# Kernel tuning notes

Hardware: AMD Instinct MI355X
Metric: run time of the kernel (lower is better)

Reference implementation:

```python
import jax, jax.numpy as jnp
import numpy as np

HID = 1024
NH = 4
DK = 256   # head_qk_dim
DV = 512   # head_v_dim
C = 64     # chunk size (fla default)
EPS = 1e-5
GLN = 16.0  # gate_logit_normalizer


def _xavier(key, shape, gain=2 ** (-2.5)):
    fan_in, fan_out = shape
    lim = gain * np.sqrt(6.0 / (fan_in + fan_out))
    return jax.random.uniform(key, shape, jnp.float32, -lim, lim)


def setup_inputs() -> dict:
    key = jax.random.key(0)
    ks = jax.random.split(key, 8)
    x = jax.random.normal(ks[0], (4, 2048, HID), jnp.float32)
    Wq = _xavier(ks[1], (HID, NH * DK))
    Wk = _xavier(ks[2], (HID, NH * DK))
    Wv = _xavier(ks[3], (HID, NH * DV))
    Wg = _xavier(ks[4], (HID, NH * DV))
    Wgk = _xavier(ks[5], (HID, NH))
    bgk = jnp.zeros((NH,), jnp.float32)
    Wo = _xavier(ks[6], (NH * DV, HID))
    gnorm_w = jnp.ones((DV,), jnp.float32)
    return {"x": x, "Wq": Wq, "Wk": Wk, "Wv": Wv, "Wg": Wg,
            "Wgk": Wgk, "bgk": bgk, "Wo": Wo, "gnorm_w": gnorm_w}


def _chunk_simple_gla(q, k, v, g):
    # q,k: [b,h,n,dk]; v: [b,h,n,dv]; g: [b,h,n] per-head scalar log-decay
    B, H, N, dk = q.shape
    dv = v.shape[-1]
    nc = N // C
    scale = dk ** -0.5
    q = q.reshape(B, H, nc, C, dk) * scale
    k = k.reshape(B, H, nc, C, dk)
    v = v.reshape(B, H, nc, C, dv)
    g = g.reshape(B, H, nc, C)
    gc = jnp.cumsum(g, axis=-1)          # inclusive within-chunk cumulative decay
    gt = gc[..., -1]                     # total chunk decay [b,h,nc]

    # intra-chunk: o[t] += sum_{s<=t} exp(gc_t - gc_s) (q_t.k_s) v_s
    dec = gc[..., :, None] - gc[..., None, :]              # [b,h,nc,C,C]
    mask = jnp.tril(jnp.ones((C, C), bool))
    A = jnp.einsum('bhntd,bhnsd->bhnts', q, k)
    A = A * jnp.where(mask, jnp.exp(jnp.where(mask, dec, 0.0)), 0.0)
    o_intra = jnp.einsum('bhnts,bhnsd->bhntd', A, v)

    # inter-chunk: carry state S [b,h,dk,dv] across chunks
    qs = jnp.moveaxis(q, 2, 0)
    ks_ = jnp.moveaxis(k, 2, 0)
    vs = jnp.moveaxis(v, 2, 0)
    gcs = jnp.moveaxis(gc, 2, 0)
    gts = jnp.moveaxis(gt, 2, 0)
    S0 = jnp.zeros((B, H, dk, dv), q.dtype)

    def step(S, inp):
        qc, kc, vc, gcc, gtc = inp
        o_int = jnp.einsum('bhtd,bhde->bhte', qc * jnp.exp(gcc)[..., None], S)
        kd = kc * jnp.exp(gtc[..., None] - gcc)[..., None]
        S = jnp.exp(gtc)[..., None, None] * S + jnp.einsum('bhtd,bhte->bhde', kd, vc)
        return S, o_int

    _, o_inter = jax.lax.scan(step, S0, (qs, ks_, vs, gcs, gts))
    o = o_intra + jnp.moveaxis(o_inter, 0, 2)
    return o.reshape(B, H, N, dv)


def reference(x, Wq, Wk, Wv, Wg, Wgk, bgk, Wo, gnorm_w):
    B, N, _ = x.shape
    q = (x @ Wq).reshape(B, N, NH, DK).transpose(0, 2, 1, 3)
    k = (x @ Wk).reshape(B, N, NH, DK).transpose(0, 2, 1, 3)
    v = (x @ Wv).reshape(B, N, NH, DV).transpose(0, 2, 1, 3)
    gk = (x @ Wgk + bgk).transpose(0, 2, 1)          # [b,h,n]
    gk = jax.nn.log_sigmoid(gk) / GLN
    o = _chunk_simple_gla(q, k, v, gk)               # [b,h,n,dv]
    o = o.transpose(0, 2, 1, 3)                      # [b,n,h,dv]
    g = (x @ Wg).reshape(B, N, NH, DV)
    # FusedRMSNormSwishGate: RMSNorm(o) * swish(g)
    on = o * jax.lax.rsqrt(jnp.mean(o * o, axis=-1, keepdims=True) + EPS) * gnorm_w
    o = on * (g * jax.nn.sigmoid(g))
    o = o.reshape(B, N, NH * DV)
    return o @ Wo
```

## Files before the change

### kernel.cpp

```cpp
#include <hip/hip_runtime.h>

constexpr int B_  = 4;
constexpr int N_  = 2048;
constexpr int HID_ = 1024;
constexpr int NH_ = 4;
constexpr int DK_ = 256;
constexpr int DV_ = 512;
constexpr int C_  = 64;
constexpr int NC_ = 32;
constexpr int M_  = B_ * N_;
constexpr int NSEG_ = 4;
constexpr int CSEG_ = NC_ / NSEG_;

using ushort_t = unsigned short;
typedef __attribute__((ext_vector_type(8))) short bf16x8;
typedef __attribute__((ext_vector_type(4))) float f32x4;

__device__ __forceinline__ ushort_t f2bf(float f) {
  union { float fv; unsigned u; } v; v.fv = f;
  unsigned r = v.u + 0x7FFFu + ((v.u >> 16) & 1u);
  return (ushort_t)(r >> 16);
}
__device__ __forceinline__ float bf2f(ushort_t u) {
  union { unsigned u; float f; } v; v.u = ((unsigned)u) << 16; return v.f;
}

__device__ __forceinline__ void gload_lds16(const void* g, void* l) {
  __builtin_amdgcn_global_load_lds(
      (const __attribute__((address_space(1))) unsigned int*)g,
      (__attribute__((address_space(3))) unsigned int*)l, 16, 0, 0);
}

__device__ __forceinline__ f32x4 mfma16(bf16x8 a, bf16x8 b, f32x4 c) {
  return __builtin_amdgcn_mfma_f32_16x16x32_bf16(a, b, c, 0, 0, 0);
}

template<bool BF16OUT>
__global__ __launch_bounds__(256) void gemm_mfma(
    const ushort_t* __restrict__ A, const ushort_t* __restrict__ BT,
    void* __restrict__ CV, int N, int K) {
  __shared__ ushort_t Asl[128 * 32];
  __shared__ ushort_t Bsl[128 * 32];
  const int tid = threadIdx.x;
  const int wave = tid >> 6, lane = tid & 63;
  const size_t brow = (size_t)blockIdx.y * 128;
  const size_t bcol = (size_t)blockIdx.x * 128;
  const int wr = (wave >> 1) * 64, wc = (wave & 1) * 64;

  f32x4 acc[4][4];
#pragma unroll
  for (int m = 0; m < 4; ++m)
#pragma unroll
    for (int n = 0; n < 4; ++n) acc[m][n] = f32x4{0.f, 0.f, 0.f, 0.f};

  const int kk   = (lane & 3) * 8;
  const int frow = lane & 15;
  const int fk   = (lane >> 4) * 8;

  for (int k0 = 0; k0 < K; k0 += 32) {
#pragma unroll
    for (int j = 0; j < 2; ++j) {
      const int cbase = j * 4 + wave;
      const int row   = (cbase * 64 + lane) >> 2;
      gload_lds16(A  + (brow + row) * K + k0 + kk, Asl + cbase * 512);
      gload_lds16(BT + (bcol + row) * K + k0 + kk, Bsl + cbase * 512);
    }
    __syncthreads();

    bf16x8 af[4], bfr[4];
#pragma unroll
    for (int m = 0; m < 4; ++m)
      af[m] = *(const bf16x8*)(Asl + (wr + m * 16 + frow) * 32 + fk);
#pragma unroll
    for (int n = 0; n < 4; ++n)
      bfr[n] = *(const bf16x8*)(Bsl + (wc + n * 16 + frow) * 32 + fk);
#pragma unroll
    for (int m = 0; m < 4; ++m)
#pragma unroll
      for (int n = 0; n < 4; ++n)
        acc[m][n] = mfma16(af[m], bfr[n], acc[m][n]);
    __syncthreads();
  }

  const int crow = (lane >> 4) * 4;
  const int ccol = lane & 15;
#pragma unroll
  for (int m = 0; m < 4; ++m)
#pragma unroll
    for (int n = 0; n < 4; ++n) {
      const size_t base = (brow + wr + m * 16 + crow) * (size_t)N + (bcol + wc + n * 16 + ccol);
      if constexpr (BF16OUT) {
        ushort_t* Out = (ushort_t*)CV;
#pragma unroll
        for (int j = 0; j < 4; ++j) Out[base + (size_t)j * N] = f2bf(acc[m][n][j]);
      } else {
        float* Out = (float*)CV;
#pragma unroll
        for (int j = 0; j < 4; ++j) Out[base + (size_t)j * N] = acc[m][n][j];
      }
    }
}

__global__ __launch_bounds__(256) void conv_to_bf16(const float* __restrict__ in,
    ushort_t* __restrict__ out) {
  const size_t i = ((size_t)blockIdx.x * 256 + threadIdx.x) * 4;
  float4 v = *(const float4*)(in + i);
  ushort4 r;
  r.x = f2bf(v.x); r.y = f2bf(v.y); r.z = f2bf(v.z); r.w = f2bf(v.w);
  *(ushort4*)(out + i) = r;
}

__global__ __launch_bounds__(256) void transp_bf16(const float* __restrict__ W,
    ushort_t* __restrict__ WT, int K, int N) {
  __shared__ float tile[32][33];
  const int n0 = blockIdx.x * 32, k0 = blockIdx.y * 32;
  const int tx = threadIdx.x & 31, ty = threadIdx.x >> 5;
#pragma unroll
  for (int i = 0; i < 32; i += 8)
    tile[ty + i][tx] = W[(size_t)(k0 + ty + i) * N + n0 + tx];
  __syncthreads();
#pragma unroll
  for (int i = 0; i < 32; i += 8)
    WT[(size_t)(n0 + ty + i) * K + k0 + tx] = f2bf(tile[tx][ty + i]);
}

__global__ __launch_bounds__(256) void gk_kernel(const float* __restrict__ x,
    const float* __restrict__ Wgk, const float* __restrict__ bgk,
    float* __restrict__ gkbuf) {
  const int row  = blockIdx.x;
  const int b    = row / N_;
  const int n    = row - b * N_;
  const int tid  = threadIdx.x;
  const int wv   = tid >> 6;
  const int ln   = tid & 63;
  __shared__ float red2[256];
  const float* xr = x + (size_t)row * HID_;
  float s = 0.f;
  for (int i = ln; i < HID_; i += 64) s += xr[i] * Wgk[i * NH_ + wv];
  red2[tid] = s;
  __syncthreads();
  for (int off = 32; off; off >>= 1) {
    if (ln < off) red2[tid] += red2[tid + off];
    __syncthreads();
  }
  if (ln == 0) {
    float z  = red2[wv * 64] + bgk[wv];
    float ls = fminf(z, 0.f) - log1pf(expf(-fabsf(z)));
    gkbuf[((size_t)(b * NH_ + wv)) * N_ + n] = ls * (1.0f / 16.0f);
  }
}

__global__ __launch_bounds__(64) void cumsum_kernel(const float* __restrict__ gkbuf,
                                                    float* __restrict__ gcbuf) {
  const int bh = blockIdx.x;
  const int c  = threadIdx.x;
  if (c < NC_) {
    const size_t base = (size_t)bh * N_ + c * C_;
    float acc = 0.f;
    for (int t = 0; t < C_; ++t) { acc += gkbuf[base + t]; gcbuf[base + t] = acc; }
  }
}

__global__ __launch_bounds__(256) void a_mfma(const ushort_t* __restrict__ qkv16,
    const float* __restrict__ gc, ushort_t* __restrict__ Abuf) {
  const int blk = blockIdx.x;
  const int bh  = blk >> 5, c = blk & 31;
  const int b   = bh >> 2, h = bh & 3;
  __shared__ float gcs[64];
  const int tid = threadIdx.x;
  const int w = tid >> 6, l = tid & 63;
  const int frow = l & 15, fgrp = l >> 4;
  if (tid < 64) gcs[tid] = gc[(size_t)bh * N_ + c * C_ + tid];
  __syncthreads();

  const size_t rbase = (size_t)(b * N_ + c * C_);
  bf16x8 aqr[8];
#pragma unroll
  for (int kk = 0; kk < 8; ++kk)
    aqr[kk] = *(const bf16x8*)(qkv16 + (rbase + w * 16 + frow) * 4096 +
                               h * 256 + kk * 32 + fgrp * 8);

  ushort_t* ab = Abuf + (size_t)blk * 4096;
  const float scl = 0.0625f;
#pragma unroll
  for (int n = 0; n < 4; ++n) {
    f32x4 acc = f32x4{0.f, 0.f, 0.f, 0.f};
#pragma unroll
    for (int kk = 0; kk < 8; ++kk) {
      bf16x8 bk = *(const bf16x8*)(qkv16 + (rbase + n * 16 + frow) * 4096 +
                                   1024 + h * 256 + kk * 32 + fgrp * 8);
      acc = mfma16(aqr[kk], bk, acc);
    }
    const int s = n * 16 + frow;
    const float gcss = gcs[s];
#pragma unroll
    for (int j = 0; j < 4; ++j) {
      const int t = w * 16 + fgrp * 4 + j;
      const float val = (s <= t) ? acc[j] * scl * expf(gcs[t] - gcss) : 0.f;
      ab[(size_t)t * 64 + s] = f2bf(val);
    }
  }
}

__global__ __launch_bounds__(256) void pack_q16(const ushort_t* __restrict__ qkv16,
    const float* __restrict__ gc, ushort_t* __restrict__ q16) {
  const size_t i8 = ((size_t)blockIdx.x * 256 + threadIdx.x) * 8;
  const int row = (int)(i8 >> 10);
  const int col = (int)(i8 & 1023);
  const int b = row >> 11, n = row & 2047;
  const int h = col >> 8;
  const float f = 0.0625f * expf(gc[(size_t)(b * NH_ + h) * N_ + n]);
  bf16x8 v = *(const bf16x8*)(qkv16 + (size_t)row * 4096 + col);
  ushort_t r[8];
#pragma unroll
  for (int j = 0; j < 8; ++j) r[j] = f2bf(bf2f((ushort_t)v[j]) * f);
  *(bf16x8*)(q16 + i8) = *(bf16x8*)r;
}

__global__ __launch_bounds__(256) void pack_kT(const ushort_t* __restrict__ qkv16,
    const float* __restrict__ gc, ushort_t* __restrict__ kT) {
  const int blk = blockIdx.x;
  const int bh = blk >> 5, c = blk & 31;
  const int b = bh >> 2, h = bh & 3;
  __shared__ ushort_t kl[256][68];
  __shared__ float fk[64];
  const int tid = threadIdx.x;
  if (tid < 64) {
    const float gct = gc[(size_t)bh * N_ + c * C_ + tid];
    const float gt  = gc[(size_t)bh * N_ + c * C_ + 63];
    fk[tid] = expf(gt - gct);
  }
  __syncthreads();
  const ushort_t* kb = qkv16 + (size_t)(b * N_ + c * C_) * 4096 + 1024 + h * 256;
  for (int it = 0; it < 8; ++it) {
    const int e = it * 256 + tid;
    const int t = e >> 5, d8 = (e & 31) * 8;
    bf16x8 kv = *(const bf16x8*)(kb + (size_t)t * 4096 + d8);
    const float f = fk[t];
#pragma unroll
    for (int j = 0; j < 8; ++j) kl[d8 + j][t] = f2bf(bf2f((ushort_t)kv[j]) * f);
  }
  __syncthreads();
  ushort_t* out = kT + (size_t)blk * 16384;
  for (int it = 0; it < 8; ++it) {
    const int e = it * 256 + tid;
    const int d = e >> 3, t8 = (e & 7) * 8;
    ushort4 lo, hi;
    lo.x = kl[d][t8 + 0]; lo.y = kl[d][t8 + 1]; lo.z = kl[d][t8 + 2]; lo.w = kl[d][t8 + 3];
    hi.x = kl[d][t8 + 4]; hi.y = kl[d][t8 + 5]; hi.z = kl[d][t8 + 6]; hi.w = kl[d][t8 + 7];
    *(ushort4*)(out + (size_t)d * 64 + t8)     = lo;
    *(ushort4*)(out + (size_t)d * 64 + t8 + 4) = hi;
  }
}

__global__ __launch_bounds__(256) void pack_vT(const ushort_t* __restrict__ qkv16,
    ushort_t* __restrict__ vT) {
  const int blk = blockIdx.x;
  const int eh = blk & 1, c = (blk >> 1) & 31, bh = blk >> 6;
  const int b = bh >> 2, h = bh & 3;
  __shared__ ushort_t vl[256][68];
  const int tid = threadIdx.x;
  const ushort_t* vb = qkv16 + (size_t)(b * N_ + c * C_) * 4096 + 2048 + h * 512 + eh * 256;
  for (int it = 0; it < 8; ++it) {
    const int e = it * 256 + tid;
    const int s = e >> 5, c8 = (e & 31) * 8;
    bf16x8 val = *(const bf16x8*)(vb + (size_t)s * 4096 + c8);
#pragma unroll
    for (int j = 0; j < 8; ++j) vl[c8 + j][s] = (ushort_t)val[j];
  }
  __syncthreads();
  ushort_t* out = vT + (size_t)bh * 512 * 2048 + (size_t)(eh * 256) * 2048 + c * C_;
  for (int it = 0; it < 8; ++it) {
    const int e = it * 256 + tid;
    const int r = e >> 3, t8 = (e & 7) * 8;
    ushort4 lo, hi;
    lo.x = vl[r][t8 + 0]; lo.y = vl[r][t8 + 1]; lo.z = vl[r][t8 + 2]; lo.w = vl[r][t8 + 3];
    hi.x = vl[r][t8 + 4]; hi.y = vl[r][t8 + 5]; hi.z = vl[r][t8 + 6]; hi.w = vl[r][t8 + 7];
    *(ushort4*)(out + (size_t)r * 2048 + t8)     = lo;
    *(ushort4*)(out + (size_t)r * 2048 + t8 + 4) = hi;
  }
}

#define LOAD_AQ(cc, dst)                                                       \
  do {                                                                         \
    _Pragma("unroll")                                                          \
    for (int kk = 0; kk < 8; ++kk)                                             \
      dst[kk] = *(const bf16x8*)(qbase + (size_t)((cc) * C_ + w * 16 + frow) * 1024 + \
                                 kk * 32 + fgrp * 8);                          \
  } while (0)

__global__ __launch_bounds__(256) void scan_mfma(
    const ushort_t* __restrict__ q16,
    const ushort_t* __restrict__ kT,
    const ushort_t* __restrict__ vT,
    const ushort_t* __restrict__ ab,
    const float*    __restrict__ gc,
    ushort_t* __restrict__ o,
    float*    __restrict__ U) {
  const int bh = blockIdx.x, vblk = blockIdx.y, sg = blockIdx.z;
  const int b = bh >> 2, h = bh & 3;
  const int e0 = vblk * 64;
  const int c0 = sg * CSEG_;
  __shared__ ushort_t sbt[2][64][264];
  __shared__ float egts[NC_];
  const int tid = threadIdx.x;
  const int w = tid >> 6, l = tid & 63;
  const int frow = l & 15, fgrp = l >> 4;

  for (int i = tid; i < 2 * 64 * 264 / 2; i += 256) ((unsigned*)&sbt[0][0][0])[i] = 0u;
  if (tid < NC_) egts[tid] = expf(gc[(size_t)bh * N_ + tid * C_ + 63]);
  f32x4 s_acc[4][4];
#pragma unroll
  for (int sm = 0; sm < 4; ++sm)
#pragma unroll
    for (int sn = 0; sn < 4; ++sn) s_acc[sm][sn] = f32x4{0.f, 0.f, 0.f, 0.f};
  __syncthreads();

  const ushort_t* qbase = q16 + (size_t)(b * N_) * 1024 + h * 256;
  const ushort_t* kbase = kT + (size_t)bh * NC_ * 16384;
  const ushort_t* vbase = vT + (size_t)bh * 512 * 2048 + (size_t)e0 * 2048;
  const ushort_t* abase = ab + (size_t)bh * NC_ * 4096;
  ushort_t*       obase = o + (size_t)(b * N_) * 2048 + h * 512 + e0;

  bf16x8 aqP[8];
  LOAD_AQ(c0, aqP);

  for (int c = c0; c < c0 + CSEG_; ++c) {
    const float egt = egts[c];
    const ushort_t (*srd)[264] = sbt[(c & 1) ^ 1];
    ushort_t (*swr)[264] = sbt[c & 1];

    bf16x8 aq[8];
#pragma unroll
    for (int kk = 0; kk < 8; ++kk) aq[kk] = aqP[kk];

    bf16x8 bv[2][4], aa[2];
#pragma unroll
    for (int kt = 0; kt < 2; ++kt)
#pragma unroll
      for (int n = 0; n < 4; ++n)
        bv[kt][n] = *(const bf16x8*)(vbase + (size_t)(n * 16 + frow) * 2048 +
                                     c * C_ + kt * 32 + fgrp * 8);
#pragma unroll
    for (int kt = 0; kt < 2; ++kt)
      aa[kt] = *(const bf16x8*)(abase + (size_t)c * 4096 + (w * 16 + frow) * 64 + kt * 32 + fgrp * 8);

#pragma unroll
    for (int n = 0; n < 4; ++n) {
      f32x4 oa = f32x4{0.f, 0.f, 0.f, 0.f};
#pragma unroll
      for (int kt = 0; kt < 2; ++kt) oa = mfma16(aa[kt], bv[kt][n], oa);
#pragma unroll
      for (int kk = 0; kk < 8; ++kk) {
        bf16x8 bs = *(const bf16x8*)(&srd[n * 16 + frow][kk * 32 + fgrp * 8]);
        oa = mfma16(aq[kk], bs, oa);
      }
#pragma unroll
      for (int j = 0; j < 4; ++j)
        obase[(size_t)(c * C_ + w * 16 + fgrp * 4 + j) * 2048 + n * 16 + frow] = f2bf(oa[j]);
    }

#pragma unroll
    for (int sm = 0; sm < 4; ++sm)
#pragma unroll
      for (int sn = 0; sn < 4; ++sn)
#pragma unroll
        for (int j = 0; j < 4; ++j) s_acc[sm][sn][j] *= egt;
#pragma unroll
    for (int kt = 0; kt < 2; ++kt)
#pragma unroll
      for (int sm = 0; sm < 4; ++sm) {
        bf16x8 ak = *(const bf16x8*)(kbase + (size_t)c * 16384 +
                                     (size_t)(w * 64 + sm * 16 + frow) * 64 + kt * 32 + fgrp * 8);
#pragma unroll
        for (int sn = 0; sn < 4; ++sn)
          s_acc[sm][sn] = mfma16(ak, bv[kt][sn], s_acc[sm][sn]);
      }

    if (c + 1 < c0 + CSEG_) LOAD_AQ(c + 1, aqP);

#pragma unroll
    for (int sm = 0; sm < 4; ++sm)
#pragma unroll
      for (int sn = 0; sn < 4; ++sn) {
        ushort4 pk;
        pk.x = f2bf(s_acc[sm][sn][0]); pk.y = f2bf(s_acc[sm][sn][1]);
        pk.z = f2bf(s_acc[sm][sn][2]); pk.w = f2bf(s_acc[sm][sn][3]);
        *(ushort4*)&swr[sn * 16 + frow][w * 64 + sm * 16 + fgrp * 4] = pk;
      }
    __syncthreads();
  }

  if (sg < NSEG_ - 1) {
    float* ub = U + (size_t)(bh * (NSEG_ - 1) + sg) * 256 * 512;
#pragma unroll
    for (int sm = 0; sm < 4; ++sm)
#pragma unroll
      for (int sn = 0; sn < 4; ++sn)
#pragma unroll
        for (int j = 0; j < 4; ++j)
          ub[(size_t)(w * 64 + sm * 16 + fgrp * 4 + j) * 512 + e0 + sn * 16 + frow] =
              s_acc[sm][sn][j];
  }
}

__global__ __launch_bounds__(256) void combine_kernel(const float* __restrict__ U,
    const float* __restrict__ gc, ushort_t* __restrict__ SinT) {
  const int bh = blockIdx.x, vb = blockIdx.y;
  const int d = threadIdx.x;
  float S[16];
#pragma unroll
  for (int e = 0; e < 16; ++e) S[e] = 0.f;
  for (int s = 0; s < NSEG_ - 1; ++s) {
    float gsum = 0.f;
    for (int c = s * CSEG_; c < (s + 1) * CSEG_; ++c)
      gsum += gc[(size_t)bh * N_ + c * C_ + 63];
    const float E = expf(gsum);
    const float* u = U + (size_t)(bh * (NSEG_ - 1) + s) * 256 * 512 + (size_t)d * 512 + vb * 16;
    ushort_t* out = SinT + (size_t)((bh * (NSEG_ - 1) + s) * 32 + vb) * 4096;
#pragma unroll
    for (int e = 0; e < 16; ++e) {
      S[e] = E * S[e] + u[e];
      out[e * 256 + d] = f2bf(S[e]);
    }
  }
}

__global__ __launch_bounds__(256) void correct_kernel(
    const ushort_t* __restrict__ q16, const ushort_t* __restrict__ SinT,
    const float* __restrict__ gc, ushort_t* __restrict__ o) {
  const int bh = blockIdx.x, vb = blockIdx.y, z = blockIdx.z;
  const int sg = z + 1, c0 = sg * CSEG_;
  const int b = bh >> 2, h = bh & 3;
  __shared__ ushort_t sT[16][264];
  __shared__ float dseg[CSEG_];
  const int tid = threadIdx.x;
  const int w = tid >> 6, l = tid & 63;
  const int frow = l & 15, fgrp = l >> 4;

  {
    const ushort_t* src = SinT + (size_t)((bh * (NSEG_ - 1) + z) * 32 + vb) * 4096;
    const int e = tid >> 4, dbase = (tid & 15) * 16;
    bf16x8 v0 = *(const bf16x8*)(src + e * 256 + dbase);
    bf16x8 v1 = *(const bf16x8*)(src + e * 256 + dbase + 8);
    *(bf16x8*)&sT[e][dbase]     = v0;
    *(bf16x8*)&sT[e][dbase + 8] = v1;
  }
  if (tid < CSEG_) {
    float s = 0.f;
    for (int i = 0; i < tid; ++i) s += gc[(size_t)bh * N_ + (c0 + i) * C_ + 63];
    dseg[tid] = expf(s);
  }
  __syncthreads();

  const ushort_t* qbase = q16 + (size_t)(b * N_) * 1024 + h * 256;
  ushort_t* obase = o + (size_t)(b * N_) * 2048 + h * 512 + vb * 16;

  for (int c = c0; c < c0 + CSEG_; ++c) {
    const float D = dseg[c - c0];
    f32x4 oa = f32x4{0.f, 0.f, 0.f, 0.f};
#pragma unroll
    for (int kk = 0; kk < 8; ++kk) {
      bf16x8 aq = *(const bf16x8*)(qbase + (size_t)(c * C_ + w * 16 + frow) * 1024 + kk * 32 + fgrp * 8);
      bf16x8 bs = *(const bf16x8*)(&sT[frow][kk * 32 + fgrp * 8]);
      oa = mfma16(aq, bs, oa);
    }
#pragma unroll
    for (int j = 0; j < 4; ++j) {
      const size_t idx = (size_t)(c * C_ + w * 16 + fgrp * 4 + j) * 2048 + frow;
      obase[idx] = f2bf(bf2f(obase[idx]) + D * oa[j]);
    }
  }
}

__global__ __launch_bounds__(256) void normgate_kernel(const ushort_t* __restrict__ o,
    const ushort_t* __restrict__ g, const float* __restrict__ w,
    ushort_t* __restrict__ ob) {
  const int blk = blockIdx.x;
  const size_t base = (size_t)blk * DV_;
  const int tid = threadIdx.x;
  __shared__ float red2[256];
  const float v0 = bf2f(o[base + tid]), v1 = bf2f(o[base + tid + 256]);
  red2[tid] = v0 * v0 + v1 * v1;
  __syncthreads();
  for (int off = 128; off; off >>= 1) {
    if (tid < off) red2[tid] += red2[tid + off];
    __syncthreads();
  }
  const float rms = rsqrtf(red2[0] * (1.0f / 512.0f) + 1e-5f);
  const float g0 = bf2f(g[base + tid]), g1 = bf2f(g[base + tid + 256]);
  const float sw0 = g0 / (1.f + expf(-g0));
  const float sw1 = g1 / (1.f + expf(-g1));
  ob[base + tid]       = f2bf(v0 * rms * w[tid] * sw0);
  ob[base + tid + 256] = f2bf(v1 * rms * w[tid + 256] * sw1);
}

extern "C" void kernel_launch(void* const* d_in, const int* in_sizes, int n_in,
                              void* d_out, int out_size, void* d_ws, size_t ws_size,
                              hipStream_t stream) {
  (void)in_sizes; (void)n_in; (void)out_size; (void)ws_size;
  const float* x    = (const float*)d_in[0];
  const float* Wq   = (const float*)d_in[1];
  const float* Wk   = (const float*)d_in[2];
  const float* Wv   = (const float*)d_in[3];
  const float* Wg   = (const float*)d_in[4];
  const float* Wgk  = (const float*)d_in[5];
  const float* bgk  = (const float*)d_in[6];
  const float* Wo   = (const float*)d_in[7];
  const float* gw   = (const float*)d_in[8];

  float* ws = (float*)d_ws;
  size_t off = 0;
  float* gk = ws + off; off += (size_t)16 * N_;
  float* gc = ws + off; off += (size_t)16 * N_;
  ushort_t* qkv16 = (ushort_t*)(ws + off); size_t qkv_off = off; off += (size_t)M_ * 4096 / 2;
  ushort_t* o    = (ushort_t*)(ws + off); off += (size_t)M_ * 2048 / 2;
  ushort_t* ab16 = (ushort_t*)(ws + off); off += (size_t)16 * NC_ * 4096 / 2;
  ushort_t* q16  = (ushort_t*)(ws + off); size_t q16_off = off; off += (size_t)M_ * 1024 / 2;
  ushort_t* kTp  = (ushort_t*)(ws + off); off += (size_t)16 * NC_ * 16384 / 2;
  ushort_t* vTp  = (ushort_t*)(ws + off); size_t vTp_off = off; off += (size_t)16 * 512 * 2048 / 2;
  ushort_t* xb   = (ushort_t*)(ws + off); off += (size_t)M_ * HID_ / 2;
  ushort_t* WqT  = (ushort_t*)(ws + off); off += (size_t)1024 * 1024 / 2;
  ushort_t* WkT  = (ushort_t*)(ws + off); off += (size_t)1024 * 1024 / 2;
  ushort_t* WvT  = (ushort_t*)(ws + off); off += (size_t)2048 * 1024 / 2;
  ushort_t* WgT  = (ushort_t*)(ws + off); off += (size_t)2048 * 1024 / 2;
  ushort_t* WoT  = (ushort_t*)(ws + off); off += (size_t)1024 * 2048 / 2;
  float*    U    = ws + qkv_off;
  ushort_t* SinT = (ushort_t*)(ws + qkv_off + 6291456);
  ushort_t* g16  = (ushort_t*)(ws + q16_off);
  ushort_t* ob   = (ushort_t*)(ws + vTp_off);

  dim3 thr(256);
  conv_to_bf16<<<M_ * HID_ / 1024, thr, 0, stream>>>(x, xb);
  transp_bf16<<<dim3(32, 32), thr, 0, stream>>>(Wq, WqT, 1024, 1024);
  transp_bf16<<<dim3(32, 32), thr, 0, stream>>>(Wk, WkT, 1024, 1024);
  transp_bf16<<<dim3(64, 32), thr, 0, stream>>>(Wv, WvT, 1024, 2048);
  transp_bf16<<<dim3(64, 32), thr, 0, stream>>>(Wg, WgT, 1024, 2048);
  transp_bf16<<<dim3(32, 64), thr, 0, stream>>>(Wo, WoT, 2048, 1024);

  gemm_mfma<true><<<dim3(32, 64), thr, 0, stream>>>(xb, WqT, qkv16, 4096, 1024);
  gk_kernel<<<M_, thr, 0, stream>>>(x, Wgk, bgk, gk);
  cumsum_kernel<<<16, 64, 0, stream>>>(gk, gc);
  a_mfma<<<16 * NC_, thr, 0, stream>>>(qkv16, gc, ab16);
  pack_q16<<<M_ * 1024 / 2048, thr, 0, stream>>>(qkv16, gc, q16);
  pack_kT<<<16 * NC_, thr, 0, stream>>>(qkv16, gc, kTp);
  pack_vT<<<16 * NC_ * 2, thr, 0, stream>>>(qkv16, vTp);
  scan_mfma<<<dim3(16, 8, NSEG_), thr, 0, stream>>>(q16, kTp, vTp, ab16, gc, o, U);
  combine_kernel<<<dim3(16, 32), thr, 0, stream>>>(U, gc, SinT);
  correct_kernel<<<dim3(16, 32, NSEG_ - 1), thr, 0, stream>>>(q16, SinT, gc, o);
  gemm_mfma<true><<<dim3(16, 64), thr, 0, stream>>>(xb, WgT, g16, 2048, 1024);
  normgate_kernel<<<M_ * NH_, thr, 0, stream>>>(o, g16, gw, ob);
  gemm_mfma<false><<<dim3(8, 64), thr, 0, stream>>>(ob, WoT, (float*)d_out, 1024, 2048);
}
```

Baseline: 476.2 us.

## Merge prep kernels, stage bf16 GEMM epilogue through LDS, prefetch scan operands

Fuses the five weight transpose/convert kernels and the x-to-bf16 conversion into one launch, which cuts launch overhead and the serialization between small kernels. The bf16 GEMM epilogue now stages the tile in shared memory so each thread writes coalesced 16-byte rows instead of scattered 2-byte stores. The scan kernel also prefetches the V and A operands for the next chunk alongside Q, hiding global load latency. In exchange the GEMM uses about 36KB more LDS, which may lower occupancy, and the scan kernel holds more registers for the prefetch buffers.

New measurement: 513.0 us. 1.08x slower.

```diff
diff --git a/kernel.cpp b/kernel.cpp
--- a/kernel.cpp
+++ b/kernel.cpp
@@ -41,6 +41,7 @@
     void* __restrict__ CV, int N, int K) {
   __shared__ ushort_t Asl[128 * 32];
   __shared__ ushort_t Bsl[128 * 32];
+  __shared__ ushort_t Csl[BF16OUT ? 128 * 144 : 1];
   const int tid = threadIdx.x;
   const int wave = tid >> 6, lane = tid & 63;
   const size_t brow = (size_t)blockIdx.y * 128;
@@ -84,40 +85,64 @@
 
   const int crow = (lane >> 4) * 4;
   const int ccol = lane & 15;
-#pragma unroll
-  for (int m = 0; m < 4; ++m)
-#pragma unroll
-    for (int n = 0; n < 4; ++n) {
-      const size_t base = (brow + wr + m * 16 + crow) * (size_t)N + (bcol + wc + n * 16 + ccol);
-      if constexpr (BF16OUT) {
-        ushort_t* Out = (ushort_t*)CV;
-#pragma unroll
-        for (int j = 0; j < 4; ++j) Out[base + (size_t)j * N] = f2bf(acc[m][n][j]);
-      } else {
-        float* Out = (float*)CV;
+  if constexpr (BF16OUT) {
+#pragma unroll
+    for (int m = 0; m < 4; ++m)
+#pragma unroll
+      for (int n = 0; n < 4; ++n)
+#pragma unroll
+        for (int j = 0; j < 4; ++j)
+          Csl[(wr + m * 16 + crow + j) * 144 + wc + n * 16 + ccol] =
+              f2bf(acc[m][n][j]);
+    __syncthreads();
+    const int orow = tid >> 1, ohalf = (tid & 1) * 64;
+    ushort_t* op = (ushort_t*)CV + (brow + orow) * (size_t)N + bcol + ohalf;
+    const ushort_t* cp = &Csl[orow * 144 + ohalf];
+#pragma unroll
+    for (int i = 0; i < 8; ++i)
+      *(bf16x8*)(op + i * 8) = *(const bf16x8*)(cp + i * 8);
+  } else {
+    float* Out = (float*)CV;
+#pragma unroll
+    for (int m = 0; m < 4; ++m)
+#pragma unroll
+      for (int n = 0; n < 4; ++n) {
+        const size_t base = (brow + wr + m * 16 + crow) * (size_t)N + (bcol + wc + n * 16 + ccol);
 #pragma unroll
         for (int j = 0; j < 4; ++j) Out[base + (size_t)j * N] = acc[m][n][j];
       }
-    }
-}
-
-__global__ __launch_bounds__(256) void conv_to_bf16(const float* __restrict__ in,
-    ushort_t* __restrict__ out) {
-  const size_t i = ((size_t)blockIdx.x * 256 + threadIdx.x) * 4;
-  float4 v = *(const float4*)(in + i);
-  ushort4 r;
-  r.x = f2bf(v.x); r.y = f2bf(v.y); r.z = f2bf(v.z); r.w = f2bf(v.w);
-  *(ushort4*)(out + i) = r;
-}
-
-__global__ __launch_bounds__(256) void transp_bf16(const float* __restrict__ W,
-    ushort_t* __restrict__ WT, int K, int N) {
+  }
+}
+
+__global__ __launch_bounds__(256) void prep_all(
+    const float* __restrict__ Wq, const float* __restrict__ Wk,
+    const float* __restrict__ Wv, const float* __restrict__ Wg,
+    const float* __restrict__ Wo, const float* __restrict__ x,
+    ushort_t* __restrict__ WqT, ushort_t* __restrict__ WkT,
+    ushort_t* __restrict__ WvT, ushort_t* __restrict__ WgT,
+    ushort_t* __restrict__ WoT, ushort_t* __restrict__ xb) {
+  const int blk = blockIdx.x;
+  const int tid = threadIdx.x;
+  if (blk >= 8192) {
+    const size_t i = ((size_t)(blk - 8192) * 1024) + tid * 4;
+    float4 v = *(const float4*)(x + i);
+    ushort4 r;
+    r.x = f2bf(v.x); r.y = f2bf(v.y); r.z = f2bf(v.z); r.w = f2bf(v.w);
+    *(ushort4*)(xb + i) = r;
+    return;
+  }
+  const float* W; ushort_t* WT; int K, Nn, gxw, local;
+  if (blk < 1024)      { W = Wq; WT = WqT; K = 1024; Nn = 1024; gxw = 32; local = blk; }
+  else if (blk < 2048) { W = Wk; WT = WkT; K = 1024; Nn = 1024; gxw = 32; local = blk - 1024; }
+  else if (blk < 4096) { W = Wv; WT = WvT; K = 1024; Nn = 2048; gxw = 64; local = blk - 2048; }
+  else if (blk < 6144) { W = Wg; WT = WgT; K = 1024; Nn = 2048; gxw = 64; local = blk - 4096; }
+  else                 { W = Wo; WT = WoT; K = 2048; Nn = 1024; gxw = 32; local = blk - 6144; }
+  const int n0 = (local % gxw) * 32, k0 = (local / gxw) * 32;
   __shared__ float tile[32][33];
-  const int n0 = blockIdx.x * 32, k0 = blockIdx.y * 32;
-  const int tx = threadIdx.x & 31, ty = threadIdx.x >> 5;
+  const int tx = tid & 31, ty = tid >> 5;
 #pragma unroll
   for (int i = 0; i < 32; i += 8)
-    tile[ty + i][tx] = W[(size_t)(k0 + ty + i) * N + n0 + tx];
+    tile[ty + i][tx] = W[(size_t)(k0 + ty + i) * Nn + n0 + tx];
   __syncthreads();
 #pragma unroll
   for (int i = 0; i < 32; i += 8)
@@ -288,6 +313,22 @@
       dst[kk] = *(const bf16x8*)(qbase + (size_t)((cc) * C_ + w * 16 + frow) * 1024 + \
                                  kk * 32 + fgrp * 8);                          \
   } while (0)
+#define LOAD_BV(cc, dst)                                                       \
+  do {                                                                         \
+    _Pragma("unroll")                                                          \
+    for (int kt = 0; kt < 2; ++kt)                                             \
+      _Pragma("unroll")                                                        \
+      for (int n = 0; n < 4; ++n)                                              \
+        dst[kt][n] = *(const bf16x8*)(vbase + (size_t)(n * 16 + frow) * 2048 + \
+                                      (cc) * C_ + kt * 32 + fgrp * 8);         \
+  } while (0)
+#define LOAD_AA(cc, dst)                                                       \
+  do {                                                                         \
+    _Pragma("unroll")                                                          \
+    for (int kt = 0; kt < 2; ++kt)                                             \
+      dst[kt] = *(const bf16x8*)(abase + (size_t)(cc) * 4096 +                 \
+                                 (w * 16 + frow) * 64 + kt * 32 + fgrp * 8);   \
+  } while (0)
 
 __global__ __launch_bounds__(256) void scan_mfma(
     const ushort_t* __restrict__ q16,
@@ -322,28 +363,25 @@
   const ushort_t* abase = ab + (size_t)bh * NC_ * 4096;
   ushort_t*       obase = o + (size_t)(b * N_) * 2048 + h * 512 + e0;
 
-  bf16x8 aqP[8];
+  bf16x8 aqP[8], bvP[2][4], aaP[2];
   LOAD_AQ(c0, aqP);
+  LOAD_BV(c0, bvP);
+  LOAD_AA(c0, aaP);
 
   for (int c = c0; c < c0 + CSEG_; ++c) {
     const float egt = egts[c];
     const ushort_t (*srd)[264] = sbt[(c & 1) ^ 1];
     ushort_t (*swr)[264] = sbt[c & 1];
 
-    bf16x8 aq[8];
+    bf16x8 aq[8], bv[2][4], aa[2];
 #pragma unroll
     for (int kk = 0; kk < 8; ++kk) aq[kk] = aqP[kk];
-
-    bf16x8 bv[2][4], aa[2];
-#pragma unroll
-    for (int kt = 0; kt < 2; ++kt)
-#pragma unroll
-      for (int n = 0; n < 4; ++n)
-        bv[kt][n] = *(const bf16x8*)(vbase + (size_t)(n * 16 + frow) * 2048 +
-                                     c * C_ + kt * 32 + fgrp * 8);
-#pragma unroll
-    for (int kt = 0; kt < 2; ++kt)
-      aa[kt] = *(const bf16x8*)(abase + (size_t)c * 4096 + (w * 16 + frow) * 64 + kt * 32 + fgrp * 8);
+#pragma unroll
+    for (int kt = 0; kt < 2; ++kt) {
+      aa[kt] = aaP[kt];
+#pragma unroll
+      for (int n = 0; n < 4; ++n) bv[kt][n] = bvP[kt][n];
+    }
 
 #pragma unroll
     for (int n = 0; n < 4; ++n) {
@@ -377,7 +415,11 @@
           s_acc[sm][sn] = mfma16(ak, bv[kt][sn], s_acc[sm][sn]);
       }
 
-    if (c + 1 < c0 + CSEG_) LOAD_AQ(c + 1, aqP);
+    if (c + 1 < c0 + CSEG_) {
+      LOAD_AQ(c + 1, aqP);
+      LOAD_BV(c + 1, bvP);
+      LOAD_AA(c + 1, aaP);
+    }
 
 #pragma unroll
     for (int sm = 0; sm < 4; ++sm)
@@ -531,12 +573,8 @@
   ushort_t* ob   = (ushort_t*)(ws + vTp_off);
 
   dim3 thr(256);
-  conv_to_bf16<<<M_ * HID_ / 1024, thr, 0, stream>>>(x, xb);
-  transp_bf16<<<dim3(32, 32), thr, 0, stream>>>(Wq, WqT, 1024, 1024);
-  transp_bf16<<<dim3(32, 32), thr, 0, stream>>>(Wk, WkT, 1024, 1024);
-  transp_bf16<<<dim3(64, 32), thr, 0, stream>>>(Wv, WvT, 1024, 2048);
-  transp_bf16<<<dim3(64, 32), thr, 0, stream>>>(Wg, WgT, 1024, 2048);
-  transp_bf16<<<dim3(32, 64), thr, 0, stream>>>(Wo, WoT, 2048, 1024);
+  prep_all<<<16384, thr, 0, stream>>>(Wq, Wk, Wv, Wg, Wo, x,
+                                      WqT, WkT, WvT, WgT, WoT, xb);
 
   gemm_mfma<true><<<dim3(32, 64), thr, 0, stream>>>(xb, WqT, qkv16, 4096, 1024);
   gk_kernel<<<M_, thr, 0, stream>>>(x, Wgk, bgk, gk);
```
